# Performance work log

Measured on AMD Instinct MI355X. Metric: run time of the kernel, lower is better.

Reference implementation:

```python
import jax, jax.numpy as jnp
import numpy as np

ALPHA = 1.702
LIMIT = 7.0
BLOCK = 32  # mxfp4 block size (values per scale)

# fp4 e2m1 lookup table, indexed by 4-bit code (sign in high bit)
FP4_LUT = jnp.array([0.0, 0.5, 1.0, 1.5, 2.0, 3.0, 4.0, 6.0,
                     -0.0, -0.5, -1.0, -1.5, -2.0, -3.0, -4.0, -6.0],
                    dtype=jnp.float32)


def dequant_mxfp4(blocks, scales):
    # blocks: [E, R, C//2] int byte values (two fp4 nibbles per byte, low nibble first)
    # scales: [E, R, C//32] e8m0 exponents; value = 2^(scale - 127)
    E, R, _ = blocks.shape
    nb = scales.shape[-1]
    lo = blocks & 0xF
    hi = (blocks >> 4) & 0xF
    vals = jnp.stack([FP4_LUT[lo], FP4_LUT[hi]], axis=-1)  # [E,R,C//2,2]
    vals = vals.reshape(E, R, nb, BLOCK)
    scale = jnp.exp2((scales - 127).astype(jnp.float32))   # [E,R,nb]
    return (vals * scale[..., None]).reshape(E, R, nb * BLOCK)  # [E,R,C]


def setup_inputs() -> dict:
    key = jax.random.key(0)
    ks = jax.random.split(key, 12)
    T, E, H, I = 1024, 8, 1024, 1024
    inp = {
        'hidden_states': jax.random.normal(ks[0], (T, H), dtype=jnp.float32),
        'router_logits': jax.random.normal(ks[1], (T, E), dtype=jnp.float32),
        'gate_proj_blocks': jax.random.randint(ks[2], (E, I, H // 2), 0, 256, dtype=jnp.int32),
        'gate_proj_scales': jax.random.randint(ks[3], (E, I, H // BLOCK), 121, 130, dtype=jnp.int32),
        'gate_proj_bias': jax.random.normal(ks[4], (E, I), dtype=jnp.float32) * 0.02,
        'up_proj_blocks': jax.random.randint(ks[5], (E, I, H // 2), 0, 256, dtype=jnp.int32),
        'up_proj_scales': jax.random.randint(ks[6], (E, I, H // BLOCK), 121, 130, dtype=jnp.int32),
        'up_proj_bias': jax.random.normal(ks[7], (E, I), dtype=jnp.float32) * 0.02,
        'down_proj_blocks': jax.random.randint(ks[8], (E, H, I // 2), 0, 256, dtype=jnp.int32),
        'down_proj_scales': jax.random.randint(ks[9], (E, H, I // BLOCK), 121, 130, dtype=jnp.int32),
        'down_proj_bias': jax.random.normal(ks[10], (E, H), dtype=jnp.float32) * 0.02,
        'k': 2,
    }
    return inp


def reference(hidden_states, router_logits, gate_proj_blocks, gate_proj_scales,
              gate_proj_bias, up_proj_blocks, up_proj_scales, up_proj_bias,
              down_proj_blocks, down_proj_scales, down_proj_bias, k):
    T, H = hidden_states.shape
    E = router_logits.shape[-1]
    # --- top-k routing: softmax over the selected logits, scattered to [T,E] ---
    top_vals, top_idx = jax.lax.top_k(router_logits, k)        # [T,k]
    top_w = jax.nn.softmax(top_vals, axis=-1)                   # [T,k]
    route = jnp.zeros((T, E), dtype=hidden_states.dtype)
    route = route.at[jnp.arange(T)[:, None], top_idx].add(top_w)  # [T,E]
    # --- dequantize mxfp4 expert weights ---
    gate_w = dequant_mxfp4(gate_proj_blocks, gate_proj_scales)  # [E,I,H]
    up_w = dequant_mxfp4(up_proj_blocks, up_proj_scales)        # [E,I,H]
    down_w = dequant_mxfp4(down_proj_blocks, down_proj_scales)  # [E,H,I]
    # --- GLU expert FFN (GPT-OSS variant) ---
    gate = jnp.einsum('th,eih->tei', hidden_states, gate_w) + gate_proj_bias[None]
    up = jnp.einsum('th,eih->tei', hidden_states, up_w) + up_proj_bias[None]
    gate = jnp.minimum(gate, LIMIT)
    up = jnp.clip(up, -LIMIT, LIMIT)
    glu = gate * jax.nn.sigmoid(gate * ALPHA)
    act = (up + 1.0) * glu                                       # [T,E,I]
    # fold routing weight in before the down projection, then sum over experts
    act = act * route[:, :, None]
    out = jnp.einsum('tei,ehi->th', act, down_w) + route @ down_proj_bias  # [T,H]
    return out
```

## Files before the change

kernel.cpp:

```cpp
#include <hip/hip_runtime.h>
#include <cstdint>
#include <cstddef>

typedef __bf16 bf16x8 __attribute__((ext_vector_type(8)));
typedef __bf16 bf16x2 __attribute__((ext_vector_type(2)));
typedef float f32x4 __attribute__((ext_vector_type(4)));
typedef unsigned short u16x2 __attribute__((ext_vector_type(2)));

constexpr int HH = 1024;
constexpr int II = 1024;
constexpr int KMAX = 2;
constexpr int EMAX = 8;
constexpr int GU_TILES = 24;
constexpr int DN_TILES = 40;
constexpr float FALPHA = 1.702f;
constexpr float FLIMIT = 7.0f;

#if __has_builtin(__builtin_amdgcn_cvt_scalef32_pk_bf16_fp4)
#define USE_CVT 1
#else
#define USE_CVT 0
#endif

#define SCHED0() __builtin_amdgcn_sched_barrier(0)

__device__ __forceinline__ unsigned pk_add16(unsigned a, unsigned b) {
  u16x2 x, y;
  __builtin_memcpy(&x, &a, 4); __builtin_memcpy(&y, &b, 4);
  u16x2 r = x + y;
  unsigned o; __builtin_memcpy(&o, &r, 4); return o;
}
__device__ __forceinline__ int4 decode_chunk(int4 raw, unsigned addk) {
  unsigned p = (unsigned)raw.x | ((unsigned)raw.y << 8) |
               ((unsigned)raw.z << 16) | ((unsigned)raw.w << 24);
  unsigned q = p >> 4;
  unsigned me = p & 0x07070707u, mo = q & 0x07070707u;
  unsigned se = p & 0x08080808u, so = q & 0x08080808u;
  unsigned hiE = __builtin_amdgcn_perm(0x40404040u, 0x3F3F3F14u, me) | (se << 4);
  unsigned hiO = __builtin_amdgcn_perm(0x40404040u, 0x3F3F3F14u, mo) | (so << 4);
  unsigned loE = __builtin_amdgcn_perm(0xC0804000u, 0xC0800000u, me);
  unsigned loO = __builtin_amdgcn_perm(0xC0804000u, 0xC0800000u, mo);
  int4 out;
  out.x = (int)pk_add16(__builtin_amdgcn_perm(hiE, loE, 0x05010400u), addk);
  out.y = (int)pk_add16(__builtin_amdgcn_perm(hiE, loE, 0x07030602u), addk);
  out.z = (int)pk_add16(__builtin_amdgcn_perm(hiO, loO, 0x05010400u), addk);
  out.w = (int)pk_add16(__builtin_amdgcn_perm(hiO, loO, 0x07030602u), addk);
  return out;
}
__device__ __forceinline__ unsigned make_addk(int s) {
  int k = s - 127;
  unsigned t = ((unsigned)(k << 7)) & 0xFFFFu;
  return t | (t << 16);
}

__device__ __forceinline__ bf16x8 decode_frag(int4 raw, int s) {
#if USE_CVT
  unsigned t0 = __builtin_amdgcn_perm((unsigned)raw.y, (unsigned)raw.x, 0x00000400u);
  unsigned t1 = __builtin_amdgcn_perm((unsigned)raw.w, (unsigned)raw.z, 0x00000400u);
  unsigned p  = __builtin_amdgcn_perm(t1, t0, 0x05040100u);
  float scf = __uint_as_float((unsigned)s << 23);
  bf16x2 a = __builtin_amdgcn_cvt_scalef32_pk_bf16_fp4(p, scf, 0);
  bf16x2 b = __builtin_amdgcn_cvt_scalef32_pk_bf16_fp4(p, scf, 1);
  bf16x2 c = __builtin_amdgcn_cvt_scalef32_pk_bf16_fp4(p, scf, 2);
  bf16x2 d = __builtin_amdgcn_cvt_scalef32_pk_bf16_fp4(p, scf, 3);
  bf16x8 r;
  r[0]=a[0]; r[1]=a[1]; r[2]=b[0]; r[3]=b[1]; r[4]=c[0]; r[5]=c[1]; r[6]=d[0]; r[7]=d[1];
  return r;
#else
  int4 d4 = decode_chunk(raw, make_addk(s));
  bf16x8 r; __builtin_memcpy(&r, &d4, 16);
  return r;
#endif
}

__device__ __forceinline__ void gll16(const void* g, void* l) {
  __builtin_amdgcn_global_load_lds(
      (const __attribute__((address_space(1))) void*)g,
      (__attribute__((address_space(3))) void*)l, 16, 0, 0);
}

__global__ void routing_kernel(const float* __restrict__ logits, const int* __restrict__ dk,
                               int T, int E, float* __restrict__ route,
                               int* __restrict__ tidx, float* __restrict__ tw) {
  int t = blockIdx.x * blockDim.x + threadIdx.x;
  if (t >= T) return;
  int kk = *dk; if (kk > KMAX) kk = KMAX; if (kk < 1) kk = 1;
  int EE = E > EMAX ? EMAX : E;
  float v[EMAX]; bool used[EMAX];
  for (int e = 0; e < EE; ++e) { v[e] = logits[t * E + e]; used[e] = false; route[t * E + e] = 0.f; }
  float tv[KMAX]; int ti[KMAX];
  for (int j = 0; j < kk; ++j) {
    float best = -3.4e38f; int bi = 0;
    for (int e = 0; e < EE; ++e) if (!used[e] && v[e] > best) { best = v[e]; bi = e; }
    used[bi] = true; tv[j] = best; ti[j] = bi;
  }
  float mx = tv[0], ssum = 0.f, wj[KMAX];
  for (int j = 0; j < kk; ++j) { wj[j] = __expf(tv[j] - mx); ssum += wj[j]; }
  for (int j = 0; j < kk; ++j) {
    float wv = wj[j] / ssum;
    route[t * E + ti[j]] = wv;
    tidx[t * kk + j] = ti[j];
    tw[t * kk + j] = wv;
  }
}

__global__ void build_lists(const int* __restrict__ tidx, const int* __restrict__ dk,
                            int T, int* __restrict__ lists, int* __restrict__ counts) {
  int e = blockIdx.x;
  int lane = threadIdx.x;
  int kk = *dk; if (kk > KMAX) kk = KMAX; if (kk < 1) kk = 1;
  int cnt = 0;
  for (int base = 0; base < T; base += 64) {
    int t = base + lane;
    int j = -1;
    if (t < T) {
      for (int q = 0; q < kk; ++q) if (tidx[t * kk + q] == e) j = q;
    }
    unsigned long long m = __ballot(j >= 0);
    if (j >= 0) {
      int pre = __popcll(m & ((1ull << lane) - 1ull));
      lists[e * T + cnt + pre] = (t << 3) | j;
    }
    cnt += __popcll(m);
  }
  if (lane == 0) counts[e] = cnt;
}

__global__ void build_tiles(const int* __restrict__ counts, int E,
                            int* __restrict__ tabGU, int* __restrict__ tabDN) {
  if (threadIdx.x == 0 && blockIdx.x == 0) {
    int g = 0, d = 0;
    for (int e = 0; e < E && e < EMAX; ++e) {
      int c = counts[e];
      for (int m = 0; m * 128 < c && g < GU_TILES; ++m) tabGU[g++] = (e << 16) | m;
      for (int m = 0; m * 64 < c && d < DN_TILES; ++m) tabDN[d++] = (e << 16) | m;
    }
    for (; g < GU_TILES; ++g) tabGU[g] = -1;
    for (; d < DN_TILES; ++d) tabDN[d] = -1;
  }
}

__global__ void convert_hs(const float* __restrict__ hs, __bf16* __restrict__ hsb, int n8) {
  int g = blockIdx.x * 256 + threadIdx.x;
  if (g >= n8) return;
  const float4* p = (const float4*)hs + (size_t)g * 2;
  float4 a = p[0], b = p[1];
  bf16x8 r;
#if USE_CVT
  r[0] = (__bf16)a.x; r[1] = (__bf16)a.y; r[2] = (__bf16)a.z; r[3] = (__bf16)a.w;
  r[4] = (__bf16)b.x; r[5] = (__bf16)b.y; r[6] = (__bf16)b.z; r[7] = (__bf16)b.w;
#else
  r[0] = (__bf16)a.x; r[1] = (__bf16)a.z; r[2] = (__bf16)b.x; r[3] = (__bf16)b.z;
  r[4] = (__bf16)a.y; r[5] = (__bf16)a.w; r[6] = (__bf16)b.y; r[7] = (__bf16)b.w;
#endif
  *(bf16x8*)(hsb + (size_t)g * 8) = r;
}

__global__ __launch_bounds__(256, 2) void gemm_gate_up(
    const __bf16* __restrict__ hsb,
    const int* __restrict__ gblk, const int* __restrict__ gscl, const float* __restrict__ gbias,
    const int* __restrict__ ublk, const int* __restrict__ uscl, const float* __restrict__ ubias,
    const int* __restrict__ lists, const int* __restrict__ counts,
    const float* __restrict__ tw, const int* __restrict__ dk,
    const int* __restrict__ tab,
    __bf16* __restrict__ act, int T)
{
  int te = tab[blockIdx.x];
  if (te < 0) return;
  int e = te >> 16, mtile = te & 0xFFFF;
  int cnt = counts[e];
  int n_valid = cnt - mtile * 128;
  if (n_valid <= 0) return;
  if (n_valid > 128) n_valid = 128;
  int kk = *dk; if (kk > KMAX) kk = KMAX; if (kk < 1) kk = 1;

  __shared__ int s_tok[128];
  __shared__ __attribute__((aligned(16))) char Abuf[2][16384];
  __shared__ __attribute__((aligned(16))) char Braw[2][16384];
  __shared__ __attribute__((aligned(8))) unsigned short sScl[2][64][36];

  int tid = threadIdx.x;
  if (tid < 128) {
    int idx = mtile * 128 + tid;
    s_tok[tid] = lists[e * T + (idx < cnt ? idx : mtile * 128)];
  }
  __syncthreads();

  int lane = tid & 63, w = tid >> 6;
  int r15 = lane & 15, kg = lane >> 4;
  int wr = w >> 1, wc = w & 1;
  int cA = (lane & 7) ^ (lane >> 3);
  int ibase = blockIdx.y * 64;

  unsigned aOff[4];
  #pragma unroll
  for (int q = 0; q < 4; ++q) {
    int row = w * 32 + q * 8 + (lane >> 3);
    int tok = s_tok[row] >> 3;
    aOff[q] = (unsigned)tok * (HH * 2) + (unsigned)cA * 16;
  }
  const char* bSrc[4];
  #pragma unroll
  for (int q = 0; q < 4; ++q) {
    int row = w * 32 + q * 8 + (lane >> 3);
    int mat = (row >> 4) & 1;
    int i = ibase + ((row >> 5) << 4) + (row & 15);
    const int* base = mat ? ublk : gblk;
    bSrc[q] = (const char*)(base + ((size_t)e * II + i) * (HH / 2)) + cA * 16;
  }

  #pragma unroll
  for (int q = 0; q < 4; ++q) {
    gll16((const char*)hsb + aOff[q], Abuf[0] + (w * 32 + q * 8) * 128);
    gll16(bSrc[q], Braw[0] + (w * 32 + q * 8) * 128);
  }
  #pragma unroll
  for (int q = 0; q < 4; ++q) {
    gll16((const char*)hsb + aOff[q] + 128, Abuf[1] + (w * 32 + q * 8) * 128);
    gll16(bSrc[q] + 128, Braw[1] + (w * 32 + q * 8) * 128);
  }

  for (int idx = tid; idx < 1024; idx += 256) {
    int sgm = idx >> 9, rem = idx & 511;
    int row = rem >> 3, c4 = rem & 7;
    const int* base = sgm ? uscl : gscl;
    int4 v = *((const int4*)(base + ((size_t)e * II + ibase + row) * 32) + c4);
    unsigned short* dst = &sScl[sgm][row][c4 * 4];
    dst[0] = (unsigned short)v.x; dst[1] = (unsigned short)v.y;
    dst[2] = (unsigned short)v.z; dst[3] = (unsigned short)v.w;
  }
  __syncthreads();

  f32x4 acc[4][4];
  #pragma unroll
  for (int a = 0; a < 4; ++a)
    #pragma unroll
    for (int b = 0; b < 4; ++b) acc[a][b] = (f32x4)0.f;

  constexpr int NK = HH / 64;
  #pragma unroll 1
  for (int t = 0; t < NK; ++t) {
    if (t > 0) {
      if (t < NK - 1) { asm volatile("s_waitcnt vmcnt(8)" ::: "memory"); }
      else            { asm volatile("s_waitcnt vmcnt(0)" ::: "memory"); }
      SCHED0();
      __builtin_amdgcn_s_barrier();
      SCHED0();
    }
    const char* Ac = Abuf[t & 1];
    const char* Bc = Braw[t & 1];
    unsigned sv[4];
    #pragma unroll
    for (int fn = 0; fn < 4; ++fn) {
      int mat = fn & 1;
      int il = (wc * 2 + (fn >> 1)) * 16 + r15;
      sv[fn] = *(const unsigned*)((const char*)sScl + (mat * 64 + il) * 72 + t * 4);
    }
    #pragma unroll
    for (int kq = 0; kq < 2; ++kq) {
      int kc = kq * 4 + kg;
      bf16x8 bfr[4];
      #pragma unroll
      for (int fn = 0; fn < 4; ++fn) {
        int n = wc * 64 + fn * 16 + r15;
        int4 raw = *(const int4*)(Bc + n * 128 + ((kc ^ (n & 7)) << 4));
        int s = kq ? (int)(sv[fn] >> 16) : (int)(sv[fn] & 0xFFFF);
        bfr[fn] = decode_frag(raw, s);
      }
      #pragma unroll
      for (int fm = 0; fm < 4; ++fm) {
        int m = wr * 64 + fm * 16 + r15;
        bf16x8 af = *(const bf16x8*)(Ac + m * 128 + ((kc ^ (m & 7)) << 4));
        #pragma unroll
        for (int fn = 0; fn < 4; ++fn)
          acc[fm][fn] = __builtin_amdgcn_mfma_f32_16x16x32_bf16(af, bfr[fn], acc[fm][fn], 0, 0, 0);
      }
    }
    if (t + 2 < NK) {
      asm volatile("s_waitcnt lgkmcnt(0)" ::: "memory");
      SCHED0();
      __builtin_amdgcn_s_barrier();
      SCHED0();
      char* An = Abuf[t & 1];
      char* Bn = Braw[t & 1];
      #pragma unroll
      for (int q = 0; q < 4; ++q) {
        gll16((const char*)hsb + aOff[q] + (t + 2) * 128, An + (w * 32 + q * 8) * 128);
        gll16(bSrc[q] + (t + 2) * 128, Bn + (w * 32 + q * 8) * 128);
      }
    }
  }

  #pragma unroll
  for (int p = 0; p < 2; ++p) {
    int i_log = ibase + wc * 32 + p * 16 + r15;
    float gb = gbias[e * II + i_log], ub = ubias[e * II + i_log];
#if USE_CVT
    int i_st = i_log;
#else
    int i_st = (i_log & ~7) | ((i_log & 1) << 2) | ((i_log & 7) >> 1);
#endif
    #pragma unroll
    for (int fm = 0; fm < 4; ++fm) {
      #pragma unroll
      for (int rg = 0; rg < 4; ++rg) {
        int mloc = wr * 64 + fm * 16 + kg * 4 + rg;
        if (mloc < n_valid) {
          int entry = s_tok[mloc];
          int t2 = entry >> 3, j = entry & 7;
          float wv = tw[t2 * kk + j];
          float g = fminf(acc[fm][p * 2][rg] + gb, FLIMIT);
          float u = fminf(fmaxf(acc[fm][p * 2 + 1][rg] + ub, -FLIMIT), FLIMIT);
          float glu = g / (1.f + __expf(-FALPHA * g));
          act[((size_t)t2 * kk + j) * II + i_st] = (__bf16)((u + 1.f) * glu * wv);
        }
      }
    }
  }
}

__global__ __launch_bounds__(256, 2) void gemm_down(
    const __bf16* __restrict__ act,
    const int* __restrict__ dblk, const int* __restrict__ dscl,
    const int* __restrict__ lists, const int* __restrict__ counts,
    const int* __restrict__ dk, const int* __restrict__ tab,
    __bf16* __restrict__ partial, int T)
{
  int te = tab[blockIdx.x];
  if (te < 0) return;
  int e = te >> 16, mtile = te & 0xFFFF;
  int cnt = counts[e];
  int n_valid = cnt - mtile * 64;
  if (n_valid <= 0) return;
  if (n_valid > 64) n_valid = 64;
  int kk = *dk; if (kk > KMAX) kk = KMAX; if (kk < 1) kk = 1;

  __shared__ int s_tok[64];
  __shared__ __attribute__((aligned(16))) char Abuf[2][8192];
  __shared__ __attribute__((aligned(16))) char Braw[2][16384];
  __shared__ __attribute__((aligned(8))) unsigned short sScl[128][36];

  int tid = threadIdx.x;
  if (tid < 64) {
    int idx = mtile * 64 + tid;
    s_tok[tid] = lists[e * T + (idx < cnt ? idx : mtile * 64)];
  }
  __syncthreads();

  int lane = tid & 63, w = tid >> 6;
  int r15 = lane & 15, kg = lane >> 4;
  int wr = w >> 1, wc = w & 1;
  int cA = (lane & 7) ^ (lane >> 3);
  int hbase = blockIdx.y * 128;

  unsigned aOff[2];
  #pragma unroll
  for (int q = 0; q < 2; ++q) {
    int row = w * 16 + q * 8 + (lane >> 3);
    int entry = s_tok[row];
    unsigned slot = (unsigned)(entry >> 3) * kk + (entry & 7);
    aOff[q] = slot * (II * 2) + (unsigned)cA * 16;
  }
  const char* bSrc[4];
  #pragma unroll
  for (int q = 0; q < 4; ++q) {
    int row = w * 32 + q * 8 + (lane >> 3);
    int h = hbase + row;
    bSrc[q] = (const char*)(dblk + ((size_t)e * HH + h) * (II / 2)) + cA * 16;
  }

  #pragma unroll
  for (int q = 0; q < 2; ++q)
    gll16((const char*)act + aOff[q], Abuf[0] + (w * 16 + q * 8) * 128);
  #pragma unroll
  for (int q = 0; q < 4; ++q)
    gll16(bSrc[q], Braw[0] + (w * 32 + q * 8) * 128);
  #pragma unroll
  for (int q = 0; q < 2; ++q)
    gll16((const char*)act + aOff[q] + 128, Abuf[1] + (w * 16 + q * 8) * 128);
  #pragma unroll
  for (int q = 0; q < 4; ++q)
    gll16(bSrc[q] + 128, Braw[1] + (w * 32 + q * 8) * 128);

  for (int idx = tid; idx < 1024; idx += 256) {
    int row = idx >> 3, c4 = idx & 7;
    int4 v = *((const int4*)(dscl + ((size_t)e * HH + hbase + row) * 32) + c4);
    unsigned short* dst = &sScl[row][c4 * 4];
    dst[0] = (unsigned short)v.x; dst[1] = (unsigned short)v.y;
    dst[2] = (unsigned short)v.z; dst[3] = (unsigned short)v.w;
  }
  __syncthreads();

  f32x4 acc[2][4];
  #pragma unroll
  for (int a = 0; a < 2; ++a)
    #pragma unroll
    for (int b = 0; b < 4; ++b) acc[a][b] = (f32x4)0.f;

  constexpr int NK = II / 64;
  #pragma unroll 1
  for (int t = 0; t < NK; ++t) {
    if (t > 0) {
      if (t < NK - 1) { asm volatile("s_waitcnt vmcnt(6)" ::: "memory"); }
      else            { asm volatile("s_waitcnt vmcnt(0)" ::: "memory"); }
      SCHED0();
      __builtin_amdgcn_s_barrier();
      SCHED0();
    }
    const char* Ac = Abuf[t & 1];
    const char* Bc = Braw[t & 1];
    unsigned sv[4];
    #pragma unroll
    for (int fn = 0; fn < 4; ++fn) {
      int n = wc * 64 + fn * 16 + r15;
      sv[fn] = *(const unsigned*)((const char*)sScl + n * 72 + t * 4);
    }
    #pragma unroll
    for (int kq = 0; kq < 2; ++kq) {
      int kc = kq * 4 + kg;
      bf16x8 bfr[4];
      #pragma unroll
      for (int fn = 0; fn < 4; ++fn) {
        int n = wc * 64 + fn * 16 + r15;
        int4 raw = *(const int4*)(Bc + n * 128 + ((kc ^ (n & 7)) << 4));
        int s = kq ? (int)(sv[fn] >> 16) : (int)(sv[fn] & 0xFFFF);
        bfr[fn] = decode_frag(raw, s);
      }
      #pragma unroll
      for (int fm = 0; fm < 2; ++fm) {
        int m = wr * 32 + fm * 16 + r15;
        bf16x8 af = *(const bf16x8*)(Ac + m * 128 + ((kc ^ (m & 7)) << 4));
        #pragma unroll
        for (int fn = 0; fn < 4; ++fn)
          acc[fm][fn] = __builtin_amdgcn_mfma_f32_16x16x32_bf16(af, bfr[fn], acc[fm][fn], 0, 0, 0);
      }
    }
    if (t + 2 < NK) {
      asm volatile("s_waitcnt lgkmcnt(0)" ::: "memory");
      SCHED0();
      __builtin_amdgcn_s_barrier();
      SCHED0();
      char* An = Abuf[t & 1];
      char* Bn = Braw[t & 1];
      #pragma unroll
      for (int q = 0; q < 2; ++q)
        gll16((const char*)act + aOff[q] + (t + 2) * 128, An + (w * 16 + q * 8) * 128);
      #pragma unroll
      for (int q = 0; q < 4; ++q)
        gll16(bSrc[q] + (t + 2) * 128, Bn + (w * 32 + q * 8) * 128);
    }
  }

  #pragma unroll
  for (int fm = 0; fm < 2; ++fm) {
    #pragma unroll
    for (int rg = 0; rg < 4; ++rg) {
      int mloc = wr * 32 + fm * 16 + kg * 4 + rg;
      if (mloc < n_valid) {
        int entry = s_tok[mloc];
        int t2 = entry >> 3, j = entry & 7;
        size_t slot = (size_t)t2 * kk + j;
        #pragma unroll
        for (int fn = 0; fn < 4; ++fn) {
          int h = hbase + wc * 64 + fn * 16 + r15;
          partial[slot * HH + h] = (__bf16)acc[fm][fn][rg];
        }
      }
    }
  }
}

__global__ void combine_kernel(const __bf16* __restrict__ partial, const float* __restrict__ route,
                               const float* __restrict__ dbias, const int* __restrict__ dk,
                               float* __restrict__ out, int E) {
  int t = blockIdx.y;
  int h = blockIdx.x * 256 + threadIdx.x;
  int kk = *dk; if (kk > KMAX) kk = KMAX; if (kk < 1) kk = 1;
  float s = 0.f;
  for (int j = 0; j < kk; ++j) s += (float)partial[((size_t)t * kk + j) * HH + h];
  for (int e = 0; e < E; ++e) s += route[t * E + e] * dbias[(size_t)e * HH + h];
  out[(size_t)t * HH + h] = s;
}

extern "C" void kernel_launch(void* const* d_in, const int* in_sizes, int n_in,
                              void* d_out, int out_size, void* d_ws, size_t ws_size,
                              hipStream_t stream) {
  const float* hs    = (const float*)d_in[0];
  const float* rl    = (const float*)d_in[1];
  const int*   gblk  = (const int*)d_in[2];
  const int*   gscl  = (const int*)d_in[3];
  const float* gbias = (const float*)d_in[4];
  const int*   ublk  = (const int*)d_in[5];
  const int*   uscl  = (const int*)d_in[6];
  const float* ubias = (const float*)d_in[7];
  const int*   dblk  = (const int*)d_in[8];
  const int*   dscl  = (const int*)d_in[9];
  const float* dbias = (const float*)d_in[10];
  const int*   dk    = (const int*)d_in[11];

  long s0 = in_sizes[0], s1 = in_sizes[1], s2 = in_sizes[2], s4 = in_sizes[4];
  int H = (int)(2 * s2 / s4);
  int T = (int)(s0 / H);
  int E = (int)(s1 / T);

  char* w = (char*)d_ws;
  auto alloc = [&](size_t bytes) { char* p = w; w += (bytes + 255) & ~size_t(255); return p; };
  float*  route   = (float*)alloc(sizeof(float) * (size_t)T * E);
  int*    tidx    = (int*)  alloc(sizeof(int)   * (size_t)T * KMAX);
  float*  twp     = (float*)alloc(sizeof(float) * (size_t)T * KMAX);
  int*    counts  = (int*)  alloc(sizeof(int)   * (size_t)E);
  int*    lists   = (int*)  alloc(sizeof(int)   * (size_t)E * T);
  int*    tabGU   = (int*)  alloc(sizeof(int)   * GU_TILES);
  int*    tabDN   = (int*)  alloc(sizeof(int)   * DN_TILES);
  __bf16* hsb     = (__bf16*)alloc(sizeof(__bf16) * (size_t)T * HH);
  __bf16* act     = (__bf16*)alloc(sizeof(__bf16) * (size_t)T * KMAX * II);
  __bf16* partial = (__bf16*)alloc(sizeof(__bf16) * (size_t)T * KMAX * HH);

  routing_kernel<<<dim3((T + 255) / 256), 256, 0, stream>>>(rl, dk, T, E, route, tidx, twp);
  build_lists<<<dim3(E), 64, 0, stream>>>(tidx, dk, T, lists, counts);
  build_tiles<<<dim3(1), 64, 0, stream>>>(counts, E, tabGU, tabDN);
  convert_hs<<<dim3((T * HH / 8 + 255) / 256), 256, 0, stream>>>(hs, hsb, T * HH / 8);
  gemm_gate_up<<<dim3(GU_TILES, II / 64), 256, 0, stream>>>(
      hsb, gblk, gscl, gbias, ublk, uscl, ubias, lists, counts, twp, dk, tabGU, act, T);
  gemm_down<<<dim3(DN_TILES, HH / 128), 256, 0, stream>>>(
      act, dblk, dscl, lists, counts, dk, tabDN, partial, T);
  combine_kernel<<<dim3(HH / 256, T), 256, 0, stream>>>(partial, route, dbias, dk, (float*)d_out, E);
}
```

Measured before the change: 92.61 us.

## Switch expert GEMMs to single-wave blocks with smaller barrier-free tiles

Both grouped GEMM kernels (gate/up and down) now run with one 64-thread wave per block instead of four waves. M and N tiles are halved, and the tile tables and grid sizes are enlarged to match. With only one wave per block, the block barriers and the shared token-index staging go away. Each lane now loads its own scale row and reads the token list directly from global memory. The aim is more blocks spread across CUs and no cross-wave synchronisation stalls. The cost is more repeated weight and activation loads per expert, because smaller tiles get less reuse.

```diff
diff --git a/kernel.cpp b/kernel.cpp
--- a/kernel.cpp
+++ b/kernel.cpp
@@ -11,8 +11,8 @@
 constexpr int II = 1024;
 constexpr int KMAX = 2;
 constexpr int EMAX = 8;
-constexpr int GU_TILES = 24;
-constexpr int DN_TILES = 40;
+constexpr int GU_TILES = 40;
+constexpr int DN_TILES = 72;
 constexpr float FALPHA = 1.702f;
 constexpr float FLIMIT = 7.0f;
 
@@ -132,8 +132,8 @@
     int g = 0, d = 0;
     for (int e = 0; e < E && e < EMAX; ++e) {
       int c = counts[e];
-      for (int m = 0; m * 128 < c && g < GU_TILES; ++m) tabGU[g++] = (e << 16) | m;
-      for (int m = 0; m * 64 < c && d < DN_TILES; ++m) tabDN[d++] = (e << 16) | m;
+      for (int m = 0; m * 64 < c && g < GU_TILES; ++m) tabGU[g++] = (e << 16) | m;
+      for (int m = 0; m * 32 < c && d < DN_TILES; ++m) tabDN[d++] = (e << 16) | m;
     }
     for (; g < GU_TILES; ++g) tabGU[g] = -1;
     for (; d < DN_TILES; ++d) tabDN[d] = -1;
@@ -156,7 +156,7 @@
   *(bf16x8*)(hsb + (size_t)g * 8) = r;
 }
 
-__global__ __launch_bounds__(256, 2) void gemm_gate_up(
+__global__ __launch_bounds__(64) void gemm_gate_up(
     const __bf16* __restrict__ hsb,
     const int* __restrict__ gblk, const int* __restrict__ gscl, const float* __restrict__ gbias,
     const int* __restrict__ ublk, const int* __restrict__ uscl, const float* __restrict__ ubias,
@@ -169,67 +169,63 @@
   if (te < 0) return;
   int e = te >> 16, mtile = te & 0xFFFF;
   int cnt = counts[e];
-  int n_valid = cnt - mtile * 128;
+  int n_valid = cnt - mtile * 64;
   if (n_valid <= 0) return;
-  if (n_valid > 128) n_valid = 128;
+  if (n_valid > 64) n_valid = 64;
   int kk = *dk; if (kk > KMAX) kk = KMAX; if (kk < 1) kk = 1;
 
-  __shared__ int s_tok[128];
-  __shared__ __attribute__((aligned(16))) char Abuf[2][16384];
-  __shared__ __attribute__((aligned(16))) char Braw[2][16384];
-  __shared__ __attribute__((aligned(8))) unsigned short sScl[2][64][36];
-
-  int tid = threadIdx.x;
-  if (tid < 128) {
-    int idx = mtile * 128 + tid;
-    s_tok[tid] = lists[e * T + (idx < cnt ? idx : mtile * 128)];
-  }
-  __syncthreads();
-
-  int lane = tid & 63, w = tid >> 6;
+  __shared__ __attribute__((aligned(16))) char Abuf[2][8192];
+  __shared__ __attribute__((aligned(16))) char Braw[2][8192];
+  __shared__ __attribute__((aligned(16))) unsigned short sS[64][40];
+
+  int lane = threadIdx.x;
   int r15 = lane & 15, kg = lane >> 4;
-  int wr = w >> 1, wc = w & 1;
-  int cA = (lane & 7) ^ (lane >> 3);
-  int ibase = blockIdx.y * 64;
-
-  unsigned aOff[4];
-  #pragma unroll
-  for (int q = 0; q < 4; ++q) {
-    int row = w * 32 + q * 8 + (lane >> 3);
-    int tok = s_tok[row] >> 3;
-    aOff[q] = (unsigned)tok * (HH * 2) + (unsigned)cA * 16;
-  }
-  const char* bSrc[4];
-  #pragma unroll
-  for (int q = 0; q < 4; ++q) {
-    int row = w * 32 + q * 8 + (lane >> 3);
+  int cA = (lane & 7) ^ ((lane >> 3) & 7);
+  int ibase = blockIdx.y * 32;
+
+  {
+    int n = lane;
+    int mat = (n >> 4) & 1;
+    int i = ibase + ((n >> 5) << 4) + (n & 15);
+    const int* sb = (mat ? uscl : gscl) + ((size_t)e * II + i) * 32;
+    #pragma unroll
+    for (int c4 = 0; c4 < 8; ++c4) {
+      int4 v = ((const int4*)sb)[c4];
+      unsigned lo = ((unsigned)v.x & 0xFFFFu) | ((unsigned)v.y << 16);
+      unsigned hi = ((unsigned)v.z & 0xFFFFu) | ((unsigned)v.w << 16);
+      *(unsigned*)((char*)&sS[n][0] + c4 * 8)     = lo;
+      *(unsigned*)((char*)&sS[n][0] + c4 * 8 + 4) = hi;
+    }
+  }
+
+  unsigned aOff[8];
+  #pragma unroll
+  for (int q = 0; q < 8; ++q) {
+    int row = q * 8 + (lane >> 3);
+    int idx = mtile * 64 + row;
+    int entry = lists[e * T + (idx < cnt ? idx : mtile * 64)];
+    aOff[q] = (unsigned)(entry >> 3) * (HH * 2) + (unsigned)cA * 16;
+  }
+  const char* bAddr[8];
+  #pragma unroll
+  for (int q = 0; q < 8; ++q) {
+    int row = q * 8 + (lane >> 3);
     int mat = (row >> 4) & 1;
     int i = ibase + ((row >> 5) << 4) + (row & 15);
     const int* base = mat ? ublk : gblk;
-    bSrc[q] = (const char*)(base + ((size_t)e * II + i) * (HH / 2)) + cA * 16;
-  }
-
-  #pragma unroll
-  for (int q = 0; q < 4; ++q) {
-    gll16((const char*)hsb + aOff[q], Abuf[0] + (w * 32 + q * 8) * 128);
-    gll16(bSrc[q], Braw[0] + (w * 32 + q * 8) * 128);
-  }
-  #pragma unroll
-  for (int q = 0; q < 4; ++q) {
-    gll16((const char*)hsb + aOff[q] + 128, Abuf[1] + (w * 32 + q * 8) * 128);
-    gll16(bSrc[q] + 128, Braw[1] + (w * 32 + q * 8) * 128);
-  }
-
-  for (int idx = tid; idx < 1024; idx += 256) {
-    int sgm = idx >> 9, rem = idx & 511;
-    int row = rem >> 3, c4 = rem & 7;
-    const int* base = sgm ? uscl : gscl;
-    int4 v = *((const int4*)(base + ((size_t)e * II + ibase + row) * 32) + c4);
-    unsigned short* dst = &sScl[sgm][row][c4 * 4];
-    dst[0] = (unsigned short)v.x; dst[1] = (unsigned short)v.y;
-    dst[2] = (unsigned short)v.z; dst[3] = (unsigned short)v.w;
-  }
-  __syncthreads();
+    bAddr[q] = (const char*)(base + ((size_t)e * II + i) * (HH / 2)) + cA * 16;
+  }
+
+  #pragma unroll
+  for (int q = 0; q < 8; ++q) {
+    gll16((const char*)hsb + aOff[q], Abuf[0] + q * 1024);
+    gll16(bAddr[q], Braw[0] + q * 1024);
+  }
+  #pragma unroll
+  for (int q = 0; q < 8; ++q) {
+    gll16((const char*)hsb + aOff[q] + 128, Abuf[1] + q * 1024);
+    gll16(bAddr[q] + 128, Braw[1] + q * 1024);
+  }
 
   f32x4 acc[4][4];
   #pragma unroll
@@ -240,36 +236,29 @@
   constexpr int NK = HH / 64;
   #pragma unroll 1
   for (int t = 0; t < NK; ++t) {
-    if (t > 0) {
-      if (t < NK - 1) { asm volatile("s_waitcnt vmcnt(8)" ::: "memory"); }
-      else            { asm volatile("s_waitcnt vmcnt(0)" ::: "memory"); }
-      SCHED0();
-      __builtin_amdgcn_s_barrier();
-      SCHED0();
-    }
+    if (t < NK - 1) { asm volatile("s_waitcnt vmcnt(16)" ::: "memory"); }
+    else            { asm volatile("s_waitcnt vmcnt(0)" ::: "memory"); }
+    SCHED0();
     const char* Ac = Abuf[t & 1];
     const char* Bc = Braw[t & 1];
     unsigned sv[4];
     #pragma unroll
-    for (int fn = 0; fn < 4; ++fn) {
-      int mat = fn & 1;
-      int il = (wc * 2 + (fn >> 1)) * 16 + r15;
-      sv[fn] = *(const unsigned*)((const char*)sScl + (mat * 64 + il) * 72 + t * 4);
-    }
+    for (int fn = 0; fn < 4; ++fn)
+      sv[fn] = *(const unsigned*)((const char*)&sS[fn * 16 + r15][0] + t * 4);
     #pragma unroll
     for (int kq = 0; kq < 2; ++kq) {
       int kc = kq * 4 + kg;
       bf16x8 bfr[4];
       #pragma unroll
       for (int fn = 0; fn < 4; ++fn) {
-        int n = wc * 64 + fn * 16 + r15;
+        int n = fn * 16 + r15;
         int4 raw = *(const int4*)(Bc + n * 128 + ((kc ^ (n & 7)) << 4));
         int s = kq ? (int)(sv[fn] >> 16) : (int)(sv[fn] & 0xFFFF);
         bfr[fn] = decode_frag(raw, s);
       }
       #pragma unroll
       for (int fm = 0; fm < 4; ++fm) {
-        int m = wr * 64 + fm * 16 + r15;
+        int m = fm * 16 + r15;
         bf16x8 af = *(const bf16x8*)(Ac + m * 128 + ((kc ^ (m & 7)) << 4));
         #pragma unroll
         for (int fn = 0; fn < 4; ++fn)
@@ -279,21 +268,19 @@
     if (t + 2 < NK) {
       asm volatile("s_waitcnt lgkmcnt(0)" ::: "memory");
       SCHED0();
-      __builtin_amdgcn_s_barrier();
-      SCHED0();
       char* An = Abuf[t & 1];
       char* Bn = Braw[t & 1];
       #pragma unroll
-      for (int q = 0; q < 4; ++q) {
-        gll16((const char*)hsb + aOff[q] + (t + 2) * 128, An + (w * 32 + q * 8) * 128);
-        gll16(bSrc[q] + (t + 2) * 128, Bn + (w * 32 + q * 8) * 128);
+      for (int q = 0; q < 8; ++q) {
+        gll16((const char*)hsb + aOff[q] + (t + 2) * 128, An + q * 1024);
+        gll16(bAddr[q] + (t + 2) * 128, Bn + q * 1024);
       }
     }
   }
 
   #pragma unroll
   for (int p = 0; p < 2; ++p) {
-    int i_log = ibase + wc * 32 + p * 16 + r15;
+    int i_log = ibase + p * 16 + r15;
     float gb = gbias[e * II + i_log], ub = ubias[e * II + i_log];
 #if USE_CVT
     int i_st = i_log;
@@ -304,9 +291,9 @@
     for (int fm = 0; fm < 4; ++fm) {
       #pragma unroll
       for (int rg = 0; rg < 4; ++rg) {
-        int mloc = wr * 64 + fm * 16 + kg * 4 + rg;
+        int mloc = fm * 16 + kg * 4 + rg;
         if (mloc < n_valid) {
-          int entry = s_tok[mloc];
+          int entry = lists[e * T + mtile * 64 + mloc];
           int t2 = entry >> 3, j = entry & 7;
           float wv = tw[t2 * kk + j];
           float g = fminf(acc[fm][p * 2][rg] + gb, FLIMIT);
@@ -319,7 +306,7 @@
   }
 }
 
-__global__ __launch_bounds__(256, 2) void gemm_down(
+__global__ __launch_bounds__(64) void gemm_down(
     const __bf16* __restrict__ act,
     const int* __restrict__ dblk, const int* __restrict__ dscl,
     const int* __restrict__ lists, const int* __restrict__ counts,
@@ -330,66 +317,57 @@
   if (te < 0) return;
   int e = te >> 16, mtile = te & 0xFFFF;
   int cnt = counts[e];
-  int n_valid = cnt - mtile * 64;
+  int n_valid = cnt - mtile * 32;
   if (n_valid <= 0) return;
-  if (n_valid > 64) n_valid = 64;
+  if (n_valid > 32) n_valid = 32;
   int kk = *dk; if (kk > KMAX) kk = KMAX; if (kk < 1) kk = 1;
 
-  __shared__ int s_tok[64];
-  __shared__ __attribute__((aligned(16))) char Abuf[2][8192];
-  __shared__ __attribute__((aligned(16))) char Braw[2][16384];
-  __shared__ __attribute__((aligned(8))) unsigned short sScl[128][36];
-
-  int tid = threadIdx.x;
-  if (tid < 64) {
-    int idx = mtile * 64 + tid;
-    s_tok[tid] = lists[e * T + (idx < cnt ? idx : mtile * 64)];
-  }
-  __syncthreads();
-
-  int lane = tid & 63, w = tid >> 6;
+  __shared__ __attribute__((aligned(16))) char Abuf[2][4096];
+  __shared__ __attribute__((aligned(16))) char Braw[2][8192];
+  __shared__ __attribute__((aligned(16))) unsigned short sS[64][40];
+
+  int lane = threadIdx.x;
   int r15 = lane & 15, kg = lane >> 4;
-  int wr = w >> 1, wc = w & 1;
-  int cA = (lane & 7) ^ (lane >> 3);
-  int hbase = blockIdx.y * 128;
-
-  unsigned aOff[2];
-  #pragma unroll
-  for (int q = 0; q < 2; ++q) {
-    int row = w * 16 + q * 8 + (lane >> 3);
-    int entry = s_tok[row];
+  int cA = (lane & 7) ^ ((lane >> 3) & 7);
+  int hbase = blockIdx.y * 64;
+
+  {
+    int n = lane;
+    const int* sb = dscl + ((size_t)e * HH + hbase + n) * 32;
+    #pragma unroll
+    for (int c4 = 0; c4 < 8; ++c4) {
+      int4 v = ((const int4*)sb)[c4];
+      unsigned lo = ((unsigned)v.x & 0xFFFFu) | ((unsigned)v.y << 16);
+      unsigned hi = ((unsigned)v.z & 0xFFFFu) | ((unsigned)v.w << 16);
+      *(unsigned*)((char*)&sS[n][0] + c4 * 8)     = lo;
+      *(unsigned*)((char*)&sS[n][0] + c4 * 8 + 4) = hi;
+    }
+  }
+
+  unsigned aOff[4];
+  #pragma unroll
+  for (int q = 0; q < 4; ++q) {
+    int row = q * 8 + (lane >> 3);
+    int idx = mtile * 32 + row;
+    int entry = lists[e * T + (idx < cnt ? idx : mtile * 32)];
     unsigned slot = (unsigned)(entry >> 3) * kk + (entry & 7);
     aOff[q] = slot * (II * 2) + (unsigned)cA * 16;
   }
-  const char* bSrc[4];
-  #pragma unroll
-  for (int q = 0; q < 4; ++q) {
-    int row = w * 32 + q * 8 + (lane >> 3);
-    int h = hbase + row;
-    bSrc[q] = (const char*)(dblk + ((size_t)e * HH + h) * (II / 2)) + cA * 16;
-  }
-
-  #pragma unroll
-  for (int q = 0; q < 2; ++q)
-    gll16((const char*)act + aOff[q], Abuf[0] + (w * 16 + q * 8) * 128);
-  #pragma unroll
-  for (int q = 0; q < 4; ++q)
-    gll16(bSrc[q], Braw[0] + (w * 32 + q * 8) * 128);
-  #pragma unroll
-  for (int q = 0; q < 2; ++q)
-    gll16((const char*)act + aOff[q] + 128, Abuf[1] + (w * 16 + q * 8) * 128);
-  #pragma unroll
-  for (int q = 0; q < 4; ++q)
-    gll16(bSrc[q] + 128, Braw[1] + (w * 32 + q * 8) * 128);
-
-  for (int idx = tid; idx < 1024; idx += 256) {
-    int row = idx >> 3, c4 = idx & 7;
-    int4 v = *((const int4*)(dscl + ((size_t)e * HH + hbase + row) * 32) + c4);
-    unsigned short* dst = &sScl[row][c4 * 4];
-    dst[0] = (unsigned short)v.x; dst[1] = (unsigned short)v.y;
-    dst[2] = (unsigned short)v.z; dst[3] = (unsigned short)v.w;
-  }
-  __syncthreads();
+  const char* bAddr[8];
+  #pragma unroll
+  for (int q = 0; q < 8; ++q) {
+    int row = q * 8 + (lane >> 3);
+    bAddr[q] = (const char*)(dblk + ((size_t)e * HH + hbase + row) * (II / 2)) + cA * 16;
+  }
+
+  #pragma unroll
+  for (int q = 0; q < 4; ++q) gll16((const char*)act + aOff[q], Abuf[0] + q * 1024);
+  #pragma unroll
+  for (int q = 0; q < 8; ++q) gll16(bAddr[q], Braw[0] + q * 1024);
+  #pragma unroll
+  for (int q = 0; q < 4; ++q) gll16((const char*)act + aOff[q] + 128, Abuf[1] + q * 1024);
+  #pragma unroll
+  for (int q = 0; q < 8; ++q) gll16(bAddr[q] + 128, Braw[1] + q * 1024);
 
   f32x4 acc[2][4];
   #pragma unroll
@@ -400,35 +378,29 @@
   constexpr int NK = II / 64;
   #pragma unroll 1
   for (int t = 0; t < NK; ++t) {
-    if (t > 0) {
-      if (t < NK - 1) { asm volatile("s_waitcnt vmcnt(6)" ::: "memory"); }
-      else            { asm volatile("s_waitcnt vmcnt(0)" ::: "memory"); }
-      SCHED0();
-      __builtin_amdgcn_s_barrier();
-      SCHED0();
-    }
+    if (t < NK - 1) { asm volatile("s_waitcnt vmcnt(12)" ::: "memory"); }
+    else            { asm volatile("s_waitcnt vmcnt(0)" ::: "memory"); }
+    SCHED0();
     const char* Ac = Abuf[t & 1];
     const char* Bc = Braw[t & 1];
     unsigned sv[4];
     #pragma unroll
-    for (int fn = 0; fn < 4; ++fn) {
-      int n = wc * 64 + fn * 16 + r15;
-      sv[fn] = *(const unsigned*)((const char*)sScl + n * 72 + t * 4);
-    }
+    for (int fn = 0; fn < 4; ++fn)
+      sv[fn] = *(const unsigned*)((const char*)&sS[fn * 16 + r15][0] + t * 4);
     #pragma unroll
     for (int kq = 0; kq < 2; ++kq) {
       int kc = kq * 4 + kg;
       bf16x8 bfr[4];
       #pragma unroll
       for (int fn = 0; fn < 4; ++fn) {
-        int n = wc * 64 + fn * 16 + r15;
+        int n = fn * 16 + r15;
         int4 raw = *(const int4*)(Bc + n * 128 + ((kc ^ (n & 7)) << 4));
         int s = kq ? (int)(sv[fn] >> 16) : (int)(sv[fn] & 0xFFFF);
         bfr[fn] = decode_frag(raw, s);
       }
       #pragma unroll
       for (int fm = 0; fm < 2; ++fm) {
-        int m = wr * 32 + fm * 16 + r15;
+        int m = fm * 16 + r15;
         bf16x8 af = *(const bf16x8*)(Ac + m * 128 + ((kc ^ (m & 7)) << 4));
         #pragma unroll
         for (int fn = 0; fn < 4; ++fn)
@@ -438,16 +410,12 @@
     if (t + 2 < NK) {
       asm volatile("s_waitcnt lgkmcnt(0)" ::: "memory");
       SCHED0();
-      __builtin_amdgcn_s_barrier();
-      SCHED0();
       char* An = Abuf[t & 1];
       char* Bn = Braw[t & 1];
       #pragma unroll
-      for (int q = 0; q < 2; ++q)
-        gll16((const char*)act + aOff[q] + (t + 2) * 128, An + (w * 16 + q * 8) * 128);
-      #pragma unroll
-      for (int q = 0; q < 4; ++q)
-        gll16(bSrc[q] + (t + 2) * 128, Bn + (w * 32 + q * 8) * 128);
+      for (int q = 0; q < 4; ++q) gll16((const char*)act + aOff[q] + (t + 2) * 128, An + q * 1024);
+      #pragma unroll
+      for (int q = 0; q < 8; ++q) gll16(bAddr[q] + (t + 2) * 128, Bn + q * 1024);
     }
   }
 
@@ -455,14 +423,14 @@
   for (int fm = 0; fm < 2; ++fm) {
     #pragma unroll
     for (int rg = 0; rg < 4; ++rg) {
-      int mloc = wr * 32 + fm * 16 + kg * 4 + rg;
+      int mloc = fm * 16 + kg * 4 + rg;
       if (mloc < n_valid) {
-        int entry = s_tok[mloc];
+        int entry = lists[e * T + mtile * 32 + mloc];
         int t2 = entry >> 3, j = entry & 7;
         size_t slot = (size_t)t2 * kk + j;
         #pragma unroll
         for (int fn = 0; fn < 4; ++fn) {
-          int h = hbase + wc * 64 + fn * 16 + r15;
+          int h = hbase + fn * 16 + r15;
           partial[slot * HH + h] = (__bf16)acc[fm][fn][rg];
         }
       }
@@ -520,9 +488,9 @@
   build_lists<<<dim3(E), 64, 0, stream>>>(tidx, dk, T, lists, counts);
   build_tiles<<<dim3(1), 64, 0, stream>>>(counts, E, tabGU, tabDN);
   convert_hs<<<dim3((T * HH / 8 + 255) / 256), 256, 0, stream>>>(hs, hsb, T * HH / 8);
-  gemm_gate_up<<<dim3(GU_TILES, II / 64), 256, 0, stream>>>(
+  gemm_gate_up<<<dim3(GU_TILES, II / 32), 64, 0, stream>>>(
       hsb, gblk, gscl, gbias, ublk, uscl, ubias, lists, counts, twp, dk, tabGU, act, T);
-  gemm_down<<<dim3(DN_TILES, HH / 128), 256, 0, stream>>>(
+  gemm_down<<<dim3(DN_TILES, HH / 64), 64, 0, stream>>>(
       act, dblk, dscl, lists, counts, dk, tabDN, partial, T);
   combine_kernel<<<dim3(HH / 256, T), 256, 0, stream>>>(partial, route, dbias, dk, (float*)d_out, E);
 }
```

Measured after the change: 120.9 us. +30.5%, slower.
